# Kernel tuning notes

Hardware: AMD Instinct MI355X
Metric: run time of the kernel (lower is better)

Reference implementation:

```python
import jax, jax.numpy as jnp
import numpy as np

BATCH, SEQ_LEN, NOISE_DIM, SEQ_DIM, HID = 8192, 256, 8, 4, 64

def setup_inputs() -> dict:
    key = jax.random.key(0)
    ks = jax.random.split(key, 6)
    s = lambda k, shp, fan: jax.random.normal(k, shp, jnp.float32) * (1.0 / np.sqrt(fan))
    return {
        "noise": jax.random.normal(ks[0], (BATCH, SEQ_LEN, NOISE_DIM), jnp.float32),
        "Wx": s(ks[1], (SEQ_DIM + NOISE_DIM, 4 * HID), SEQ_DIM + NOISE_DIM),
        "Wh": s(ks[2], (HID, 4 * HID), HID),
        "b": jnp.zeros((4 * HID,), jnp.float32),
        "W1": s(ks[3], (HID, HID), HID), "b1": jnp.zeros((HID,), jnp.float32),
        "W2": s(ks[4], (HID, HID), HID), "b2": jnp.zeros((HID,), jnp.float32),
        "W3": s(ks[5], (HID, SEQ_DIM), HID), "b3": jnp.zeros((SEQ_DIM,), jnp.float32),
    }

def reference(noise, Wx, Wh, b, W1, b1, W2, b2, W3, b3):
    batch = noise.shape[0]
    # log_series=True -> initial x is zeros
    x0 = jnp.zeros((batch, SEQ_DIM), noise.dtype)
    h0 = jnp.zeros((batch, HID), noise.dtype)
    c0 = jnp.zeros((batch, HID), noise.dtype)
    noise_t = jnp.swapaxes(noise[:, : SEQ_LEN - 1, :], 0, 1)  # [L-1, B, noise_dim]

    def step(carry, n_t):
        x, h, c = carry
        inp = jnp.concatenate([x, n_t], axis=-1)           # [B, seq_dim+noise_dim]
        z = inp @ Wx + h @ Wh + b                          # [B, 4H], keras gate order i,f,g,o
        i, f, g, o = jnp.split(z, 4, axis=-1)
        c = jax.nn.sigmoid(f) * c + jax.nn.sigmoid(i) * jnp.tanh(g)
        h = jax.nn.sigmoid(o) * jnp.tanh(c)
        y = jax.nn.relu(h @ W1 + b1)
        y = jax.nn.relu(y @ W2 + b2)
        x_new = y @ W3 + b3                                # [B, seq_dim]
        return (x_new, h, c), x_new

    _, xs = jax.lax.scan(step, (x0, h0, c0), noise_t)       # [L-1, B, seq_dim]
    seq = jnp.concatenate([x0[None], xs], axis=0)           # [L, B, seq_dim]
    seq = jnp.swapaxes(seq, 0, 1)                           # [B, L, seq_dim]
    return jnp.cumsum(seq, axis=1)
```

## Files before the change

kernel.cpp:

```cpp
#include <hip/hip_runtime.h>


typedef _Float16 h8 __attribute__((ext_vector_type(8)));
typedef float f4 __attribute__((ext_vector_type(4)));

#define MFMA(a, b, c) __builtin_amdgcn_mfma_f32_16x16x32_f16(a, b, c, 0, 0, 0)

constexpr int SEQ = 256, STEPS = 255, ND = 8, SD = 4, HID = 64, G4 = 256;
constexpr int UST = 104;
constexpr int YST = 72;

__device__ __forceinline__ float sigf(float x) {
    return __builtin_amdgcn_rcpf(1.0f + __expf(-x));
}
__device__ __forceinline__ float tanh_(float x) {
    return 2.0f * __builtin_amdgcn_rcpf(1.0f + __expf(-2.0f * x)) - 1.0f;
}

__global__ __launch_bounds__(256, 2) void genlstm_kernel(
    const float* __restrict__ noise, const float* __restrict__ Wx,
    const float* __restrict__ Wh, const float* __restrict__ b,
    const float* __restrict__ W1, const float* __restrict__ b1,
    const float* __restrict__ W2, const float* __restrict__ b2,
    const float* __restrict__ W3, const float* __restrict__ b3,
    float* __restrict__ out)
{
    __shared__ _Float16 Ubuf[2][16 * UST];
    __shared__ _Float16 Y1[16 * YST];
    __shared__ _Float16 Y2[16 * YST];

    const int tid  = threadIdx.x;
    const int wid  = tid >> 6;
    const int lane = tid & 63;
    const int col  = lane & 15;
    const int quad = lane >> 4;
    const int q8   = quad * 8;
    const int row0 = blockIdx.x * 16;
    const int n0   = wid * 16 + col;

    h8 wg[4][3], w1f[2], w2f[2], w3f[2];
    #pragma unroll
    for (int g = 0; g < 4; ++g)
        #pragma unroll
        for (int s = 0; s < 3; ++s)
            #pragma unroll
            for (int j = 0; j < 8; ++j) {
                const int k = 32 * s + q8 + j;
                const int n = 64 * g + n0;
                float v = 0.0f;
                if (k < 12) v = Wx[k * G4 + n];
                else if (k >= 16 && k < 80) v = Wh[(k - 16) * G4 + n];
                wg[g][s][j] = (_Float16)v;
            }
    #pragma unroll
    for (int s = 0; s < 2; ++s)
        #pragma unroll
        for (int j = 0; j < 8; ++j) {
            const int k = 32 * s + q8 + j;
            w1f[s][j] = (_Float16)W1[k * HID + n0];
            w2f[s][j] = (_Float16)W2[k * HID + n0];
            w3f[s][j] = (_Float16)(col < 4 ? W3[k * SD + col] : 0.0f);
        }
    float bz[4];
    #pragma unroll
    for (int g = 0; g < 4; ++g) bz[g] = b[64 * g + n0];
    const float b1v = b1[n0], b2v = b2[n0];
    const float b3v = (col < 4) ? b3[col] : 0.0f;

    {
        _Float16* ub = &Ubuf[0][0];
        for (int i = tid; i < 2 * 16 * UST; i += 256) ub[i] = (_Float16)0.0f;
    }
    __syncthreads();
    const int nrow = lane >> 2, ncc = (lane & 3) * 2;
    if (wid == 1) {
        float2 nz = *(const float2*)(noise + ((size_t)(row0 + nrow) * SEQ + 0) * ND + ncc);
        Ubuf[0][nrow * UST + 4 + ncc] = (_Float16)nz.x;
        Ubuf[0][nrow * UST + 5 + ncc] = (_Float16)nz.y;
    }
    if (wid == 0 && lane < 16) {
        float4 z; z.x = z.y = z.z = z.w = 0.0f;
        *(float4*)(out + ((size_t)(row0 + lane) * SEQ) * SD) = z;
    }
    __syncthreads();

    float cst[4] = {0.0f, 0.0f, 0.0f, 0.0f};
    float run[4] = {0.0f, 0.0f, 0.0f, 0.0f};
    int pc = 0;

    #pragma unroll 1
    for (int t = 0; t < STEPS; ++t) {
        _Float16* Uc = &Ubuf[pc][0];
        _Float16* Un = &Ubuf[pc ^ 1][0];

        float2 nz;
        if (wid == 1)
            nz = *(const float2*)(noise + ((size_t)(row0 + nrow) * SEQ + (t + 1)) * ND + ncc);

        const _Float16* Umc = Uc + col * UST;
        h8 a0 = *(const h8*)(Umc + q8);
        h8 a1 = *(const h8*)(Umc + 32 + q8);
        h8 a2 = *(const h8*)(Umc + 64 + q8);

        f4 za[4];
        #pragma unroll
        for (int g = 0; g < 4; ++g) za[g] = (f4){bz[g], bz[g], bz[g], bz[g]};
        #pragma unroll
        for (int g = 0; g < 4; ++g) {
            za[g] = MFMA(a0, wg[g][0], za[g]);
            za[g] = MFMA(a1, wg[g][1], za[g]);
            za[g] = MFMA(a2, wg[g][2], za[g]);
        }
        #pragma unroll
        for (int r = 0; r < 4; ++r) {
            float I  = sigf(za[0][r]);
            float F  = sigf(za[1][r]);
            float G  = tanh_(za[2][r]);
            float O  = sigf(za[3][r]);
            float cn = F * cst[r] + I * G;
            cst[r] = cn;
            float H = O * tanh_(cn);
            Un[(quad * 4 + r) * UST + 16 + n0] = (_Float16)H;
        }
        __syncthreads();

        const _Float16* Umn = Un + col * UST;
        h8 hh0 = *(const h8*)(Umn + 16 + q8);
        h8 hh1 = *(const h8*)(Umn + 48 + q8);
        f4 y1a = {b1v, b1v, b1v, b1v};
        y1a = MFMA(hh0, w1f[0], y1a);
        y1a = MFMA(hh1, w1f[1], y1a);
        #pragma unroll
        for (int r = 0; r < 4; ++r)
            Y1[(quad * 4 + r) * YST + n0] = (_Float16)fmaxf(y1a[r], 0.0f);
        __syncthreads();

        const _Float16* Y1m = Y1 + col * YST;
        h8 ya0 = *(const h8*)(Y1m + q8);
        h8 ya1 = *(const h8*)(Y1m + 32 + q8);
        f4 y2a = {b2v, b2v, b2v, b2v};
        y2a = MFMA(ya0, w2f[0], y2a);
        y2a = MFMA(ya1, w2f[1], y2a);
        #pragma unroll
        for (int r = 0; r < 4; ++r)
            Y2[(quad * 4 + r) * YST + n0] = (_Float16)fmaxf(y2a[r], 0.0f);
        __syncthreads();

        if (wid == 0) {
            const _Float16* Y2m = Y2 + col * YST;
            h8 yb0 = *(const h8*)(Y2m + q8);
            h8 yb1 = *(const h8*)(Y2m + 32 + q8);
            f4 xa = {b3v, b3v, b3v, b3v};
            xa = MFMA(yb0, w3f[0], xa);
            xa = MFMA(yb1, w3f[1], xa);
            if (col < 4) {
                #pragma unroll
                for (int r = 0; r < 4; ++r) {
                    run[r] += xa[r];
                    out[((size_t)(row0 + quad * 4 + r) * SEQ + (t + 1)) * SD + col] = run[r];
                    Un[(quad * 4 + r) * UST + col] = (_Float16)xa[r];
                }
            }
        }
        if (wid == 1) {
            Un[nrow * UST + 4 + ncc] = (_Float16)nz.x;
            Un[nrow * UST + 5 + ncc] = (_Float16)nz.y;
        }
        __syncthreads();
        pc ^= 1;
    }
}

extern "C" void kernel_launch(void* const* d_in, const int* in_sizes, int n_in,
                              void* d_out, int out_size, void* d_ws, size_t ws_size,
                              hipStream_t stream) {
    genlstm_kernel<<<512, 256, 0, stream>>>(
        (const float*)d_in[0], (const float*)d_in[1], (const float*)d_in[2],
        (const float*)d_in[3], (const float*)d_in[4], (const float*)d_in[5],
        (const float*)d_in[6], (const float*)d_in[7], (const float*)d_in[8],
        (const float*)d_in[9], (float*)d_out);
}
```

Baseline: 425.2 us.

## Process two row groups per block, transpose MFMA operands, drop a barrier per step

Each block now handles 32 batch rows as two independent 16-row groups, with 256 blocks instead of 512. The MFMA operands are swapped so each lane holds four consecutive hidden units, which allows packed half-precision stores. The x/noise input is kept in per-wave private buffers so the end-of-step barrier can be removed, and the H buffer is double-buffered. The intent is to amortise barriers and interleave two independent dependency chains for latency hiding, at the cost of halving the grid and dropping occupancy to one block per CU.

```diff
diff --git a/kernel.cpp b/kernel.cpp
--- a/kernel.cpp
+++ b/kernel.cpp
@@ -2,13 +2,14 @@
 
 
 typedef _Float16 h8 __attribute__((ext_vector_type(8)));
+typedef __fp16 p2h __attribute__((ext_vector_type(2)));
 typedef float f4 __attribute__((ext_vector_type(4)));
 
 #define MFMA(a, b, c) __builtin_amdgcn_mfma_f32_16x16x32_f16(a, b, c, 0, 0, 0)
 
 constexpr int SEQ = 256, STEPS = 255, ND = 8, SD = 4, HID = 64, G4 = 256;
-constexpr int UST = 104;
-constexpr int YST = 72;
+constexpr int HST  = 72;
+constexpr int A2ST = 24;
 
 __device__ __forceinline__ float sigf(float x) {
     return __builtin_amdgcn_rcpf(1.0f + __expf(-x));
@@ -16,8 +17,20 @@
 __device__ __forceinline__ float tanh_(float x) {
     return 2.0f * __builtin_amdgcn_rcpf(1.0f + __expf(-2.0f * x)) - 1.0f;
 }
-
-__global__ __launch_bounds__(256, 2) void genlstm_kernel(
+__device__ __forceinline__ void store4h(_Float16* p, f4 v) {
+    p2h lo = __builtin_amdgcn_cvt_pkrtz(v[0], v[1]);
+    p2h hi = __builtin_amdgcn_cvt_pkrtz(v[2], v[3]);
+    float2 st;
+    st.x = __builtin_bit_cast(float, lo);
+    st.y = __builtin_bit_cast(float, hi);
+    *(float2*)p = st;
+}
+__device__ __forceinline__ void store2h(_Float16* p, float a, float b_) {
+    p2h v = __builtin_amdgcn_cvt_pkrtz(a, b_);
+    *(float*)p = __builtin_bit_cast(float, v);
+}
+
+__global__ __launch_bounds__(256, 1) void genlstm_kernel(
     const float* __restrict__ noise, const float* __restrict__ Wx,
     const float* __restrict__ Wh, const float* __restrict__ b,
     const float* __restrict__ W1, const float* __restrict__ b1,
@@ -25,18 +38,18 @@
     const float* __restrict__ W3, const float* __restrict__ b3,
     float* __restrict__ out)
 {
-    __shared__ _Float16 Ubuf[2][16 * UST];
-    __shared__ _Float16 Y1[16 * YST];
-    __shared__ _Float16 Y2[16 * YST];
-
-    const int tid  = threadIdx.x;
-    const int wid  = tid >> 6;
-    const int lane = tid & 63;
-    const int col  = lane & 15;
-    const int quad = lane >> 4;
-    const int q8   = quad * 8;
-    const int row0 = blockIdx.x * 16;
-    const int n0   = wid * 16 + col;
+    __shared__ alignas(16) _Float16 Hb[2 * 2 * 16 * HST];
+    __shared__ alignas(16) _Float16 Y1b[2 * 16 * HST];
+    __shared__ alignas(16) _Float16 Y2b[2 * 16 * HST];
+    __shared__ alignas(16) _Float16 A2b[4 * 2 * 16 * A2ST];
+    __shared__ alignas(16) _Float16 Zb[8];
+
+    const int tid = threadIdx.x, wid = tid >> 6, lane = tid & 63;
+    const int col = lane & 15, quad = lane >> 4, q8 = quad * 8;
+    const int row0 = blockIdx.x * 32;
+    const int n0 = wid * 16 + col;
+    const int mrow = quad * 4;
+    const int wq = wid * 16 + mrow;
 
     h8 wg[4][3], w1f[2], w2f[2], w3f[2];
     #pragma unroll
@@ -47,9 +60,10 @@
             for (int j = 0; j < 8; ++j) {
                 const int k = 32 * s + q8 + j;
                 const int n = 64 * g + n0;
-                float v = 0.0f;
-                if (k < 12) v = Wx[k * G4 + n];
-                else if (k >= 16 && k < 80) v = Wh[(k - 16) * G4 + n];
+                float v;
+                if (k < 64) v = Wh[k * G4 + n];
+                else if (k < 76) v = Wx[(k - 64) * G4 + n];
+                else v = 0.0f;
                 wg[g][s][j] = (_Float16)v;
             }
     #pragma unroll
@@ -61,120 +75,150 @@
             w2f[s][j] = (_Float16)W2[k * HID + n0];
             w3f[s][j] = (_Float16)(col < 4 ? W3[k * SD + col] : 0.0f);
         }
-    float bz[4];
-    #pragma unroll
-    for (int g = 0; g < 4; ++g) bz[g] = b[64 * g + n0];
-    const float b1v = b1[n0], b2v = b2[n0];
-    const float b3v = (col < 4) ? b3[col] : 0.0f;
-
-    {
-        _Float16* ub = &Ubuf[0][0];
-        for (int i = tid; i < 2 * 16 * UST; i += 256) ub[i] = (_Float16)0.0f;
+    f4 bzv[4], b1v, b2v, b3v;
+    #pragma unroll
+    for (int r = 0; r < 4; ++r) {
+        #pragma unroll
+        for (int g = 0; g < 4; ++g) bzv[g][r] = b[64 * g + wq + r];
+        b1v[r] = b1[wq + r];
+        b2v[r] = b2[wq + r];
+        b3v[r] = (quad == 0) ? b3[r] : 0.0f;
+    }
+
+    for (int i = tid; i < 2 * 2 * 16 * HST; i += 256) Hb[i] = (_Float16)0;
+    for (int i = tid; i < 4 * 2 * 16 * A2ST; i += 256) A2b[i] = (_Float16)0;
+    if (tid < 8) Zb[tid] = (_Float16)0;
+    if (tid < 32) {
+        float4 z; z.x = z.y = z.z = z.w = 0.0f;
+        *(float4*)(out + (size_t)(row0 + tid) * SEQ * SD) = z;
     }
     __syncthreads();
+
     const int nrow = lane >> 2, ncc = (lane & 3) * 2;
-    if (wid == 1) {
-        float2 nz = *(const float2*)(noise + ((size_t)(row0 + nrow) * SEQ + 0) * ND + ncc);
-        Ubuf[0][nrow * UST + 4 + ncc] = (_Float16)nz.x;
-        Ubuf[0][nrow * UST + 5 + ncc] = (_Float16)nz.y;
-    }
-    if (wid == 0 && lane < 16) {
-        float4 z; z.x = z.y = z.z = z.w = 0.0f;
-        *(float4*)(out + ((size_t)(row0 + lane) * SEQ) * SD) = z;
-    }
-    __syncthreads();
-
-    float cst[4] = {0.0f, 0.0f, 0.0f, 0.0f};
-    float run[4] = {0.0f, 0.0f, 0.0f, 0.0f};
-    int pc = 0;
-
-    #pragma unroll 1
-    for (int t = 0; t < STEPS; ++t) {
-        _Float16* Uc = &Ubuf[pc][0];
-        _Float16* Un = &Ubuf[pc ^ 1][0];
-
-        float2 nz;
-        if (wid == 1)
-            nz = *(const float2*)(noise + ((size_t)(row0 + nrow) * SEQ + (t + 1)) * ND + ncc);
-
-        const _Float16* Umc = Uc + col * UST;
-        h8 a0 = *(const h8*)(Umc + q8);
-        h8 a1 = *(const h8*)(Umc + 32 + q8);
-        h8 a2 = *(const h8*)(Umc + 64 + q8);
-
-        f4 za[4];
-        #pragma unroll
-        for (int g = 0; g < 4; ++g) za[g] = (f4){bz[g], bz[g], bz[g], bz[g]};
-        #pragma unroll
-        for (int g = 0; g < 4; ++g) {
-            za[g] = MFMA(a0, wg[g][0], za[g]);
-            za[g] = MFMA(a1, wg[g][1], za[g]);
-            za[g] = MFMA(a2, wg[g][2], za[g]);
-        }
-        #pragma unroll
-        for (int r = 0; r < 4; ++r) {
-            float I  = sigf(za[0][r]);
-            float F  = sigf(za[1][r]);
-            float G  = tanh_(za[2][r]);
-            float O  = sigf(za[3][r]);
-            float cn = F * cst[r] + I * G;
-            cst[r] = cn;
-            float H = O * tanh_(cn);
-            Un[(quad * 4 + r) * UST + 16 + n0] = (_Float16)H;
+    const float* nptr[2];
+    _Float16* a2n[2];
+    _Float16* a2x[2];
+    const _Float16* a2rd[2];
+    _Float16* Hrow[2][2];
+    _Float16* Y1row[2];
+    _Float16* Y2row[2];
+    float* outp[2];
+    #pragma unroll
+    for (int g = 0; g < 2; ++g) {
+        nptr[g] = noise + ((size_t)(row0 + 16 * g + nrow) * SEQ) * ND + ncc;
+        a2n[g] = &A2b[((wid * 2 + g) * 16 + nrow) * A2ST + 4 + ncc];
+        a2x[g] = &A2b[((wid * 2 + g) * 16 + col) * A2ST];
+        a2rd[g] = (quad < 2) ? &A2b[((wid * 2 + g) * 16 + col) * A2ST + 8 * quad] : Zb;
+        Y1row[g] = &Y1b[(g * 16 + col) * HST];
+        Y2row[g] = &Y2b[(g * 16 + col) * HST];
+        outp[g] = out + ((size_t)(row0 + 16 * g + col) * SEQ + 1) * SD;
+        #pragma unroll
+        for (int pb = 0; pb < 2; ++pb)
+            Hrow[pb][g] = &Hb[((pb * 2 + g) * 16 + col) * HST];
+    }
+    #pragma unroll
+    for (int g = 0; g < 2; ++g) {
+        float2 nz = *(const float2*)nptr[g];
+        store2h(a2n[g], nz.x, nz.y);
+        nptr[g] += ND;
+    }
+
+    f4 cst[2], run[2];
+    #pragma unroll
+    for (int g = 0; g < 2; ++g)
+        #pragma unroll
+        for (int r = 0; r < 4; ++r) { cst[g][r] = 0.0f; run[g][r] = 0.0f; }
+
+    auto body = [&](int pb) {
+        float2 nz0 = *(const float2*)nptr[0];
+        float2 nz1 = *(const float2*)nptr[1];
+        nptr[0] += ND; nptr[1] += ND;
+
+        #pragma unroll
+        for (int g = 0; g < 2; ++g) {
+            const _Float16* hr = Hrow[pb][g];
+            h8 a0 = *(const h8*)(hr + q8);
+            h8 a1 = *(const h8*)(hr + 32 + q8);
+            h8 a2 = *(const h8*)(a2rd[g]);
+            f4 zi = bzv[0], zf = bzv[1], zg = bzv[2], zo = bzv[3];
+            zi = MFMA(wg[0][0], a0, zi); zi = MFMA(wg[0][1], a1, zi); zi = MFMA(wg[0][2], a2, zi);
+            zf = MFMA(wg[1][0], a0, zf); zf = MFMA(wg[1][1], a1, zf); zf = MFMA(wg[1][2], a2, zf);
+            zg = MFMA(wg[2][0], a0, zg); zg = MFMA(wg[2][1], a1, zg); zg = MFMA(wg[2][2], a2, zg);
+            zo = MFMA(wg[3][0], a0, zo); zo = MFMA(wg[3][1], a1, zo); zo = MFMA(wg[3][2], a2, zo);
+            f4 hv;
+            #pragma unroll
+            for (int r = 0; r < 4; ++r) {
+                float I = sigf(zi[r]), F = sigf(zf[r]);
+                float G = tanh_(zg[r]), O = sigf(zo[r]);
+                float cn = F * cst[g][r] + I * G;
+                cst[g][r] = cn;
+                hv[r] = O * tanh_(cn);
+            }
+            store4h(Hrow[pb ^ 1][g] + wq, hv);
         }
         __syncthreads();
 
-        const _Float16* Umn = Un + col * UST;
-        h8 hh0 = *(const h8*)(Umn + 16 + q8);
-        h8 hh1 = *(const h8*)(Umn + 48 + q8);
-        f4 y1a = {b1v, b1v, b1v, b1v};
-        y1a = MFMA(hh0, w1f[0], y1a);
-        y1a = MFMA(hh1, w1f[1], y1a);
-        #pragma unroll
-        for (int r = 0; r < 4; ++r)
-            Y1[(quad * 4 + r) * YST + n0] = (_Float16)fmaxf(y1a[r], 0.0f);
+        #pragma unroll
+        for (int g = 0; g < 2; ++g) {
+            const _Float16* hr = Hrow[pb ^ 1][g];
+            h8 h0 = *(const h8*)(hr + q8);
+            h8 h1 = *(const h8*)(hr + 32 + q8);
+            f4 y = b1v;
+            y = MFMA(w1f[0], h0, y);
+            y = MFMA(w1f[1], h1, y);
+            #pragma unroll
+            for (int r = 0; r < 4; ++r) y[r] = fmaxf(y[r], 0.0f);
+            store4h(Y1row[g] + wq, y);
+        }
         __syncthreads();
 
-        const _Float16* Y1m = Y1 + col * YST;
-        h8 ya0 = *(const h8*)(Y1m + q8);
-        h8 ya1 = *(const h8*)(Y1m + 32 + q8);
-        f4 y2a = {b2v, b2v, b2v, b2v};
-        y2a = MFMA(ya0, w2f[0], y2a);
-        y2a = MFMA(ya1, w2f[1], y2a);
-        #pragma unroll
-        for (int r = 0; r < 4; ++r)
-            Y2[(quad * 4 + r) * YST + n0] = (_Float16)fmaxf(y2a[r], 0.0f);
+        #pragma unroll
+        for (int g = 0; g < 2; ++g) {
+            const _Float16* yr = Y1row[g];
+            h8 p0 = *(const h8*)(yr + q8);
+            h8 p1 = *(const h8*)(yr + 32 + q8);
+            f4 y = b2v;
+            y = MFMA(w2f[0], p0, y);
+            y = MFMA(w2f[1], p1, y);
+            #pragma unroll
+            for (int r = 0; r < 4; ++r) y[r] = fmaxf(y[r], 0.0f);
+            store4h(Y2row[g] + wq, y);
+        }
         __syncthreads();
 
-        if (wid == 0) {
-            const _Float16* Y2m = Y2 + col * YST;
-            h8 yb0 = *(const h8*)(Y2m + q8);
-            h8 yb1 = *(const h8*)(Y2m + 32 + q8);
-            f4 xa = {b3v, b3v, b3v, b3v};
-            xa = MFMA(yb0, w3f[0], xa);
-            xa = MFMA(yb1, w3f[1], xa);
-            if (col < 4) {
-                #pragma unroll
-                for (int r = 0; r < 4; ++r) {
-                    run[r] += xa[r];
-                    out[((size_t)(row0 + quad * 4 + r) * SEQ + (t + 1)) * SD + col] = run[r];
-                    Un[(quad * 4 + r) * UST + col] = (_Float16)xa[r];
+        #pragma unroll
+        for (int g = 0; g < 2; ++g) {
+            const _Float16* yr = Y2row[g];
+            h8 p0 = *(const h8*)(yr + q8);
+            h8 p1 = *(const h8*)(yr + 32 + q8);
+            f4 x = b3v;
+            x = MFMA(w3f[0], p0, x);
+            x = MFMA(w3f[1], p1, x);
+            if (quad == 0) {
+                store4h(a2x[g], x);
+                if (wid == 0) {
+                    run[g] += x;
+                    *(f4*)outp[g] = run[g];
                 }
             }
-        }
-        if (wid == 1) {
-            Un[nrow * UST + 4 + ncc] = (_Float16)nz.x;
-            Un[nrow * UST + 5 + ncc] = (_Float16)nz.y;
-        }
-        __syncthreads();
-        pc ^= 1;
-    }
+            outp[g] += SD;
+        }
+        store2h(a2n[0], nz0.x, nz0.y);
+        store2h(a2n[1], nz1.x, nz1.y);
+    };
+
+    #pragma unroll 1
+    for (int t = 0; t < STEPS - 1; t += 2) {
+        body(0);
+        body(1);
+    }
+    body(0);
 }
 
 extern "C" void kernel_launch(void* const* d_in, const int* in_sizes, int n_in,
                               void* d_out, int out_size, void* d_ws, size_t ws_size,
                               hipStream_t stream) {
-    genlstm_kernel<<<512, 256, 0, stream>>>(
+    genlstm_kernel<<<256, 256, 0, stream>>>(
         (const float*)d_in[0], (const float*)d_in[1], (const float*)d_in[2],
         (const float*)d_in[3], (const float*)d_in[4], (const float*)d_in[5],
         (const float*)d_in[6], (const float*)d_in[7], (const float*)d_in[8],
```

Result: slower. 526.3 us (+23.8%).
